# Kernel optimization log

Hardware: AMD Instinct MI355X
Metric: run time of the kernel (lower is better)

Reference implementation:

```python
import jax, jax.numpy as jnp
import numpy as np

IN_CH = 256
OUT_CH = 256
NUM_HEADS = 4
LOCAL_RADIUS = 2
SCALE = OUT_CH ** 0.5  # torch divides by out_channels**0.5


def setup_inputs() -> dict:
    key = jax.random.key(0)
    ks = jax.random.split(key, 7)
    B, C, H, W = 1, IN_CH, 48, 48
    x = jax.random.normal(ks[0], (B, C, H, W), dtype=jnp.float32)
    s = 0.02
    Wq = jax.random.normal(ks[1], (OUT_CH, IN_CH), dtype=jnp.float32) * s
    Wk = jax.random.normal(ks[2], (OUT_CH, IN_CH), dtype=jnp.float32) * s
    Wv = jax.random.normal(ks[3], (OUT_CH, IN_CH), dtype=jnp.float32) * s
    bq = jax.random.normal(ks[4], (OUT_CH,), dtype=jnp.float32) * s
    bk = jax.random.normal(ks[5], (OUT_CH,), dtype=jnp.float32) * s
    bv = jax.random.normal(ks[6], (OUT_CH,), dtype=jnp.float32) * s
    return {"x": x, "Wq": Wq, "bq": bq, "Wk": Wk, "bk": bk, "Wv": Wv, "bv": bv}


def reference(x, Wq, bq, Wk, bk, Wv, bv):
    B, C, H, W = x.shape
    N = H * W
    # Faithful to torch: x.view(B, N, -1) is a raw reshape of [B,C,H,W]
    xr = x.reshape(B, N, C)
    q = xr @ Wq.T + bq  # [B, N, OUT_CH]
    k = xr @ Wk.T + bk
    v = xr @ Wv.T + bv
    dh = OUT_CH // NUM_HEADS
    # [B, heads, N, dh]
    q = q.reshape(B, N, NUM_HEADS, dh).transpose(0, 2, 1, 3)
    k = k.reshape(B, N, NUM_HEADS, dh).transpose(0, 2, 1, 3)
    v = v.reshape(B, N, NUM_HEADS, dh).transpose(0, 2, 1, 3)
    acc = jnp.zeros_like(v)
    for h in range(-LOCAL_RADIUS, LOCAL_RADIUS + 1):
        for w in range(-LOCAL_RADIUS, LOCAL_RADIUS + 1):
            # torch rolls dims (-3, -2) of [B, heads, N, dh] -> axes (1, 2)
            rk = jnp.roll(k, shift=(h, w), axis=(1, 2))
            scores = jnp.einsum('bhnd,bhmd->bhnm', q, rk) / SCALE
            p = jax.nn.softmax(scores, axis=-1)  # dropout p=0 -> identity
            rv = jnp.roll(v, shift=(-h, -w), axis=(1, 2))
            acc = acc + jnp.einsum('bhnm,bhmd->bhnd', p, rv)
    out = acc.transpose(0, 2, 1, 3).reshape(B, N, NUM_HEADS * dh)
    return out
```

## Files before the change

### kernel.cpp

```cpp
#include <hip/hip_runtime.h>


#define N_TOK 2304
#define OUTC 256
#define HSZ (N_TOK * 64)

typedef _Float16 half8 __attribute__((ext_vector_type(8)));
typedef _Float16 half4 __attribute__((ext_vector_type(4)));
typedef __fp16 fp16x2 __attribute__((ext_vector_type(2)));
typedef float f32x4 __attribute__((ext_vector_type(4)));

typedef __attribute__((address_space(3))) unsigned int as3_u32;
typedef __attribute__((address_space(1))) unsigned int as1_u32;

__device__ __forceinline__ f32x4 mfma16(half8 a, half8 b, f32x4 c) {
  return __builtin_amdgcn_mfma_f32_16x16x32_f16(a, b, c, 0, 0, 0);
}

__device__ __forceinline__ void gload_lds16(const _Float16* g, _Float16* l) {
  __builtin_amdgcn_global_load_lds((const as1_u32*)g, (as3_u32*)l, 16, 0, 0);
}

union H8U { half8 h8; fp16x2 h2[4]; };

__device__ __forceinline__ half8 pack_f32x8(const float* e) {
  H8U u;
  u.h2[0] = __builtin_amdgcn_cvt_pkrtz(e[0], e[1]);
  u.h2[1] = __builtin_amdgcn_cvt_pkrtz(e[2], e[3]);
  u.h2[2] = __builtin_amdgcn_cvt_pkrtz(e[4], e[5]);
  u.h2[3] = __builtin_amdgcn_cvt_pkrtz(e[6], e[7]);
  return u.h8;
}

__global__ __launch_bounds__(256) void k_proj(
    const float* __restrict__ x, const float* __restrict__ Wq,
    const float* __restrict__ Wk, const float* __restrict__ Wv,
    const float* __restrict__ bq, const float* __restrict__ bk,
    const float* __restrict__ bv,
    _Float16* __restrict__ Qh, _Float16* __restrict__ KF, float* __restrict__ VfT) {
  const int w = threadIdx.x >> 6, lane = threadIdx.x & 63;
  const int lr = lane & 15, lk = lane >> 4;
  const int n0 = blockIdx.x * 64 + w * 16;
  const int o0 = blockIdx.y * 64;
  const int mat = blockIdx.z;
  const float* W = (mat == 0) ? Wq : (mat == 1) ? Wk : Wv;
  f32x4 acc[4] = {};
  const float* xrow = x + (size_t)(n0 + lr) * OUTC + 8 * lk;
#pragma unroll
  for (int kk = 0; kk < 8; ++kk) {
    float af[8];
    *(float4*)&af[0] = *(const float4*)(xrow + 32 * kk);
    *(float4*)&af[4] = *(const float4*)(xrow + 32 * kk + 4);
    half8 a = pack_f32x8(af);
#pragma unroll
    for (int c = 0; c < 4; ++c) {
      const float* wrow = W + (size_t)(o0 + 16*c + lr) * OUTC + 32*kk + 8*lk;
      float bf[8];
      *(float4*)&bf[0] = *(const float4*)(wrow);
      *(float4*)&bf[4] = *(const float4*)(wrow + 4);
      half8 b = pack_f32x8(bf);
      acc[c] = mfma16(a, b, acc[c]);
    }
  }
  const float* bias = (mat == 0) ? bq : (mat == 1) ? bk : bv;
  const int hd = blockIdx.y;
#pragma unroll
  for (int c = 0; c < 4; ++c) {
    int o = o0 + 16*c + lr;
    float bo = bias[o];
    if (mat == 2) {
      float4 vv;
      vv.x = acc[c][0] + bo; vv.y = acc[c][1] + bo;
      vv.z = acc[c][2] + bo; vv.w = acc[c][3] + bo;
      *(float4*)(VfT + (size_t)o * N_TOK + n0 + 4*lk) = vv;
    } else if (mat == 0) {
      int d = 16*c + lr;
      const float qs = 0.0625f * 1.4426950408889634f;
#pragma unroll
      for (int r = 0; r < 4; ++r) {
        int n = n0 + 4*lk + r;
        Qh[((size_t)hd * N_TOK + n) * 64 + d] = (_Float16)((acc[c][r] + bo) * qs);
      }
    } else {
      int d = 16*c + lr;
      int h = d >> 5, g4K = (d >> 3) & 3, iiK = d & 7;
#pragma unroll
      for (int r = 0; r < 4; ++r) {
        int n = n0 + 4*lk + r;
        int tK = n >> 6, cK = (n >> 4) & 3, lrK = n & 15;
        KF[(size_t)hd * HSZ + ((tK*4 + cK)*2 + h)*512 + (g4K*16 + lrK)*8 + iiK] =
            (_Float16)(acc[c][r] + bo);
      }
    }
  }
}

__global__ __launch_bounds__(256) void k_smooth(
    const float* __restrict__ VfT, _Float16* __restrict__ VF) {
  const int t = blockIdx.x, vh = blockIdx.y;
  for (int f = threadIdx.x; f < 512; f += 256) {
    int cc = f >> 7, h = (f >> 6) & 1, g4 = (f >> 4) & 3, lr = f & 15;
    const float* src = VfT + (size_t)(vh*64 + 16*cc + lr) * N_TOK;
    int jbase = t*64 + 32*h + 4*g4;
    half8 out;
#pragma unroll
    for (int i = 0; i < 8; ++i) {
      int j = jbase + 16*(i >> 2) + (i & 3);
      float s = 0.f;
#pragma unroll
      for (int w = -4; w <= 4; w += 2) s += src[(j + w + N_TOK) % N_TOK];
      out[i] = (_Float16)s;
    }
    *(half8*)(VF + (size_t)vh * HSZ + (size_t)t * 4096 + f * 8) = out;
  }
}

__global__ __launch_bounds__(256, 2) void k_flash(
    const _Float16* __restrict__ Qh, const _Float16* __restrict__ KF,
    const _Float16* __restrict__ VF,
    _Float16* __restrict__ Opart, float* __restrict__ Lpart) {
  __shared__ __align__(16) _Float16 lds[2][8192];
  const int wv = threadIdx.x >> 6, lane = threadIdx.x & 63;
  const int lr = lane & 15, g4 = lane >> 4;
  const int strip = blockIdx.x * 4 + wv;
  const int n0 = strip * 32;
  const int pair = blockIdx.y;
  const int hd = pair >> 2, gk = pair & 3;
  const int chunk = blockIdx.z;
  const int vh = (2*hd + 4 - gk) & 3;

  const _Float16* Qp = Qh + ((size_t)hd * N_TOK + n0 + lr) * 64 + 8*g4;
  const half8 qa0 = *(const half8*)(Qp);
  const half8 qa1 = *(const half8*)(Qp + 32);
  const half8 qb0 = *(const half8*)(Qp + 16*64);
  const half8 qb1 = *(const half8*)(Qp + 16*64 + 32);

  const _Float16* Kt = KF + (size_t)gk * HSZ + (size_t)chunk * 9 * 4096;
  const _Float16* Vt = VF + (size_t)vh * HSZ + (size_t)chunk * 9 * 4096;
  const _Float16* gsrc = (wv < 2 ? Kt : Vt) + (wv & 1) * 2048 + lane * 8;
  const int ldsoff = (wv < 2 ? 0 : 4096) + (wv & 1) * 2048;

  f32x4 accA[4] = {}, accB[4] = {};
  f32x4 acclA = {}, acclB = {};
  half8 ones;
#pragma unroll
  for (int i = 0; i < 8; ++i) ones[i] = (_Float16)1.0f;

  auto stage = [&](int t, int b) {
    const _Float16* s = gsrc + (size_t)t * 4096;
    _Float16* d = &lds[b][ldsoff];
    gload_lds16(s,        d);
    gload_lds16(s + 512,  d + 512);
    gload_lds16(s + 1024, d + 1024);
    gload_lds16(s + 1536, d + 1536);
  };
  auto body = [&](int b) {
    const _Float16* ldsK = &lds[b][0]    + lane * 8;
    const _Float16* ldsV = &lds[b][4096] + lane * 8;
    f32x4 sA[4], sB[4];
    __builtin_amdgcn_s_setprio(1);
#pragma unroll
    for (int c = 0; c < 4; ++c) {
      half8 k0 = *(const half8*)(ldsK + c*1024);
      half8 k1 = *(const half8*)(ldsK + c*1024 + 512);
      f32x4 tA = {}; tA = mfma16(k0, qa0, tA); tA = mfma16(k1, qa1, tA); sA[c] = tA;
      f32x4 tB = {}; tB = mfma16(k0, qb0, tB); tB = mfma16(k1, qb1, tB); sB[c] = tB;
    }
    __builtin_amdgcn_s_setprio(0);
    H8U a0, a1, b0, b1;
#pragma unroll
    for (int c = 0; c < 4; ++c) {
      float eA0 = __builtin_amdgcn_exp2f(sA[c][0]);
      float eA1 = __builtin_amdgcn_exp2f(sA[c][1]);
      float eA2 = __builtin_amdgcn_exp2f(sA[c][2]);
      float eA3 = __builtin_amdgcn_exp2f(sA[c][3]);
      float eB0 = __builtin_amdgcn_exp2f(sB[c][0]);
      float eB1 = __builtin_amdgcn_exp2f(sB[c][1]);
      float eB2 = __builtin_amdgcn_exp2f(sB[c][2]);
      float eB3 = __builtin_amdgcn_exp2f(sB[c][3]);
      H8U* da = (c < 2) ? &a0 : &a1;
      H8U* db = (c < 2) ? &b0 : &b1;
      int base = (c & 1) * 2;
      da->h2[base]     = __builtin_amdgcn_cvt_pkrtz(eA0, eA1);
      da->h2[base + 1] = __builtin_amdgcn_cvt_pkrtz(eA2, eA3);
      db->h2[base]     = __builtin_amdgcn_cvt_pkrtz(eB0, eB1);
      db->h2[base + 1] = __builtin_amdgcn_cvt_pkrtz(eB2, eB3);
    }
    __builtin_amdgcn_s_setprio(1);
#pragma unroll
    for (int cc = 0; cc < 4; ++cc) {
      half8 v0 = *(const half8*)(ldsV + cc*1024);
      half8 v1 = *(const half8*)(ldsV + cc*1024 + 512);
      accA[cc] = mfma16(v0, a0.h8, accA[cc]); accA[cc] = mfma16(v1, a1.h8, accA[cc]);
      accB[cc] = mfma16(v0, b0.h8, accB[cc]); accB[cc] = mfma16(v1, b1.h8, accB[cc]);
    }
    acclA = mfma16(ones, a0.h8, acclA); acclA = mfma16(ones, a1.h8, acclA);
    acclB = mfma16(ones, b0.h8, acclB); acclB = mfma16(ones, b1.h8, acclB);
    __builtin_amdgcn_s_setprio(0);
  };

  stage(0, 0);
#pragma unroll 1
  for (int t = 0; t < 9; ++t) {
    if (t < 8) {
      stage(t + 1, (t + 1) & 1);
      asm volatile("s_waitcnt vmcnt(4)" ::: "memory");
    } else {
      asm volatile("s_waitcnt vmcnt(0)" ::: "memory");
    }
    __builtin_amdgcn_sched_barrier(0);
    __builtin_amdgcn_s_barrier();
    __builtin_amdgcn_sched_barrier(0);
    body(t & 1);
    if (t < 8) {
      __builtin_amdgcn_sched_barrier(0);
      __builtin_amdgcn_s_barrier();
    }
  }

  float invA = 1.0f / acclA[0];
  float invB = 1.0f / acclB[0];
  _Float16* Oa = Opart + (((size_t)chunk * 16 + pair) * N_TOK + n0 + lr) * 64;
  _Float16* Ob = Oa + 16 * 64;
#pragma unroll
  for (int cc = 0; cc < 4; ++cc) {
    half4 ha, hb;
#pragma unroll
    for (int r = 0; r < 4; ++r) {
      ha[r] = (_Float16)(accA[cc][r] * invA);
      hb[r] = (_Float16)(accB[cc][r] * invB);
    }
    *(half4*)(Oa + 16*cc + 4*g4) = ha;
    *(half4*)(Ob + 16*cc + 4*g4) = hb;
  }
  if (g4 == 0) {
    Lpart[((size_t)chunk * 16 + pair) * N_TOK + n0 + lr] = acclA[0];
    Lpart[((size_t)chunk * 16 + pair) * N_TOK + n0 + 16 + lr] = acclB[0];
  }
}

__global__ __launch_bounds__(256) void k_combine(
    const _Float16* __restrict__ Opart, const float* __restrict__ Lpart,
    float* __restrict__ out) {
  int gid = blockIdx.x * 256 + threadIdx.x;
  int hd = gid / (N_TOK * 8);
  int rem = gid % (N_TOK * 8);
  int n = rem >> 3, db = (rem & 7) * 8;
  float acc[8] = {};
#pragma unroll
  for (int gk = 0; gk < 4; ++gk) {
    float cg = (((hd - gk) & 3) == 2) ? 2.0f : 1.0f;
    int pair = hd * 4 + gk;
    float la[4], lsum = 0.f;
#pragma unroll
    for (int ch = 0; ch < 4; ++ch) {
      la[ch] = Lpart[((size_t)ch * 16 + pair) * N_TOK + n];
      lsum += la[ch];
    }
    float rs = cg / lsum;
#pragma unroll
    for (int ch = 0; ch < 4; ++ch) {
      half8 v = *(const half8*)(Opart + (((size_t)ch * 16 + pair) * N_TOK + n) * 64 + db);
      float w = la[ch] * rs;
#pragma unroll
      for (int i = 0; i < 8; ++i) acc[i] += w * (float)v[i];
    }
  }
  float* dst = out + (size_t)n * OUTC + hd * 64 + db;
  float4 r0, r1;
  r0.x = acc[0]; r0.y = acc[1]; r0.z = acc[2]; r0.w = acc[3];
  r1.x = acc[4]; r1.y = acc[5]; r1.z = acc[6]; r1.w = acc[7];
  *(float4*)(dst)     = r0;
  *(float4*)(dst + 4) = r1;
}

extern "C" void kernel_launch(void* const* d_in, const int* in_sizes, int n_in,
                              void* d_out, int out_size, void* d_ws, size_t ws_size,
                              hipStream_t stream) {
  (void)in_sizes; (void)n_in; (void)out_size; (void)ws_size;
  const float* x  = (const float*)d_in[0];
  const float* Wq = (const float*)d_in[1];
  const float* bq = (const float*)d_in[2];
  const float* Wk = (const float*)d_in[3];
  const float* bk = (const float*)d_in[4];
  const float* Wv = (const float*)d_in[5];
  const float* bv = (const float*)d_in[6];

  char* ws = (char*)d_ws;
  float*    Lp  = (float*)   (ws);
  _Float16* Qh  = (_Float16*)(ws + 1179648);
  _Float16* KF  = (_Float16*)(ws + 2359296);
  float*    VfT = (float*)   (ws + 3538944);
  _Float16* VF  = (_Float16*)(ws + 5898240);
  _Float16* Op  = (_Float16*)(ws + 7077888);
  float* out = (float*)d_out;

  k_proj   <<<dim3(36, 4, 3), dim3(256), 0, stream>>>(x, Wq, Wk, Wv, bq, bk, bv, Qh, KF, VfT);
  k_smooth <<<dim3(36, 4), dim3(256), 0, stream>>>(VfT, VF);
  k_flash  <<<dim3(18, 16, 4), dim3(256), 0, stream>>>(Qh, KF, VF, Op, Lp);
  k_combine<<<dim3(288), dim3(256), 0, stream>>>(Op, Lp, out);
}
```

Before: 69.12 us.

## Stage projection outputs and smoothing window in LDS for coalesced access

The projection kernel now writes Q and K tiles into shared memory first and then copies them out with contiguous 16-byte stores, replacing scattered 2-byte global stores. The smoothing kernel loads a 64x72 halo tile of V into shared memory once, so the five-tap sum reads from LDS instead of repeating strided global reads with modulo indexing. The flash kernel's launch-bounds occupancy hint is also relaxed. These add shared-memory use and a barrier per block, and dropping the occupancy hint may change register allocation in the main attention kernel.

```diff
diff --git a/kernel.cpp b/kernel.cpp
--- a/kernel.cpp
+++ b/kernel.cpp
@@ -38,6 +38,7 @@
     const float* __restrict__ bq, const float* __restrict__ bk,
     const float* __restrict__ bv,
     _Float16* __restrict__ Qh, _Float16* __restrict__ KF, float* __restrict__ VfT) {
+  __shared__ _Float16 stg[4096];
   const int w = threadIdx.x >> 6, lane = threadIdx.x & 63;
   const int lr = lane & 15, lk = lane >> 4;
   const int n0 = blockIdx.x * 64 + w * 16;
@@ -64,58 +65,78 @@
   }
   const float* bias = (mat == 0) ? bq : (mat == 1) ? bk : bv;
   const int hd = blockIdx.y;
-#pragma unroll
-  for (int c = 0; c < 4; ++c) {
-    int o = o0 + 16*c + lr;
-    float bo = bias[o];
-    if (mat == 2) {
+
+  if (mat == 2) {
+#pragma unroll
+    for (int c = 0; c < 4; ++c) {
+      int o = o0 + 16*c + lr;
+      float bo = bias[o];
       float4 vv;
       vv.x = acc[c][0] + bo; vv.y = acc[c][1] + bo;
       vv.z = acc[c][2] + bo; vv.w = acc[c][3] + bo;
       *(float4*)(VfT + (size_t)o * N_TOK + n0 + 4*lk) = vv;
-    } else if (mat == 0) {
+    }
+    return;
+  }
+
+  if (mat == 0) {
+    const float qs = 0.0625f * 1.4426950408889634f;
+#pragma unroll
+    for (int c = 0; c < 4; ++c) {
+      float bo = bias[o0 + 16*c + lr];
       int d = 16*c + lr;
-      const float qs = 0.0625f * 1.4426950408889634f;
-#pragma unroll
-      for (int r = 0; r < 4; ++r) {
-        int n = n0 + 4*lk + r;
-        Qh[((size_t)hd * N_TOK + n) * 64 + d] = (_Float16)((acc[c][r] + bo) * qs);
-      }
-    } else {
+#pragma unroll
+      for (int r = 0; r < 4; ++r)
+        stg[(w*16 + 4*lk + r) * 64 + d] = (_Float16)((acc[c][r] + bo) * qs);
+    }
+    __syncthreads();
+    _Float16* dst = Qh + ((size_t)hd * N_TOK + blockIdx.x * 64) * 64;
+    ((half8*)dst)[threadIdx.x]       = ((const half8*)stg)[threadIdx.x];
+    ((half8*)dst)[256 + threadIdx.x] = ((const half8*)stg)[256 + threadIdx.x];
+  } else {
+#pragma unroll
+    for (int c = 0; c < 4; ++c) {
+      float bo = bias[o0 + 16*c + lr];
       int d = 16*c + lr;
       int h = d >> 5, g4K = (d >> 3) & 3, iiK = d & 7;
 #pragma unroll
-      for (int r = 0; r < 4; ++r) {
-        int n = n0 + 4*lk + r;
-        int tK = n >> 6, cK = (n >> 4) & 3, lrK = n & 15;
-        KF[(size_t)hd * HSZ + ((tK*4 + cK)*2 + h)*512 + (g4K*16 + lrK)*8 + iiK] =
-            (_Float16)(acc[c][r] + bo);
-      }
-    }
+      for (int r = 0; r < 4; ++r)
+        stg[(w*2 + h)*512 + (g4K*16 + 4*lk + r)*8 + iiK] = (_Float16)(acc[c][r] + bo);
+    }
+    __syncthreads();
+    _Float16* dst = KF + (size_t)hd * HSZ + (size_t)blockIdx.x * 4096;
+    ((half8*)dst)[threadIdx.x]       = ((const half8*)stg)[threadIdx.x];
+    ((half8*)dst)[256 + threadIdx.x] = ((const half8*)stg)[256 + threadIdx.x];
   }
 }
 
 __global__ __launch_bounds__(256) void k_smooth(
     const float* __restrict__ VfT, _Float16* __restrict__ VF) {
+  __shared__ float Ls[64][76];
   const int t = blockIdx.x, vh = blockIdx.y;
+  for (int idx = threadIdx.x; idx < 64 * 72; idx += 256) {
+    int rr = idx / 72, cc = idx % 72;
+    int j = t*64 - 4 + cc; j = (j + N_TOK) % N_TOK;
+    Ls[rr][cc] = VfT[(size_t)(vh*64 + rr) * N_TOK + j];
+  }
+  __syncthreads();
   for (int f = threadIdx.x; f < 512; f += 256) {
     int cc = f >> 7, h = (f >> 6) & 1, g4 = (f >> 4) & 3, lr = f & 15;
-    const float* src = VfT + (size_t)(vh*64 + 16*cc + lr) * N_TOK;
-    int jbase = t*64 + 32*h + 4*g4;
+    int row = 16*cc + lr;
+    int base = 4 + 32*h + 4*g4;
     half8 out;
 #pragma unroll
     for (int i = 0; i < 8; ++i) {
-      int j = jbase + 16*(i >> 2) + (i & 3);
-      float s = 0.f;
-#pragma unroll
-      for (int w = -4; w <= 4; w += 2) s += src[(j + w + N_TOK) % N_TOK];
+      int loc = base + 16*(i >> 2) + (i & 3);
+      float s = Ls[row][loc-4] + Ls[row][loc-2] + Ls[row][loc]
+              + Ls[row][loc+2] + Ls[row][loc+4];
       out[i] = (_Float16)s;
     }
     *(half8*)(VF + (size_t)vh * HSZ + (size_t)t * 4096 + f * 8) = out;
   }
 }
 
-__global__ __launch_bounds__(256, 2) void k_flash(
+__global__ __launch_bounds__(256) void k_flash(
     const _Float16* __restrict__ Qh, const _Float16* __restrict__ KF,
     const _Float16* __restrict__ VF,
     _Float16* __restrict__ Opart, float* __restrict__ Lpart) {
```

Result: faster. 67.74 us (-2.0%).
